# Kernel tuning notes

Measured on AMD Instinct MI355X. Metric: run time of the kernel, lower is better.

## Reference

```python
import jax, jax.numpy as jnp
import numpy as np

# Dimensions (match init_kwargs / input_specs)
B, C, H, W = 4, 64, 96, 96
G = 4                # groups of the deformable conv
K = 3                # kernel size
PAD, STRIDE, DIL = 1, 1, 1
KK = K * K


def setup_inputs() -> dict:
    key = jax.random.key(0)
    k1, k2, k3, k4 = jax.random.split(key, 4)
    x = jax.random.normal(k1, (B, C, H, W), jnp.float32)
    # offset-predicting conv: Conv2d(C -> 2*K*K, 3x3), kaiming-ish scale
    w_off = jax.random.normal(k2, (2 * KK, C, K, K), jnp.float32) / np.sqrt(C * KK)
    b_off = jax.random.normal(k3, (2 * KK,), jnp.float32) * 0.01
    # deformable conv weight: [C_out=C, C_in/groups, K, K], bias=False
    w_def = jax.random.normal(k4, (C, C // G, K, K), jnp.float32) / np.sqrt((C // G) * KK)
    return {"x": x, "w_off": w_off, "b_off": b_off, "w_def": w_def}


def _offset_conv(x, w, b):
    y = jax.lax.conv_general_dilated(
        x, w,
        window_strides=(STRIDE, STRIDE),
        padding=((PAD, PAD), (PAD, PAD)),
        rhs_dilation=(DIL, DIL),
        dimension_numbers=("NCHW", "OIHW", "NCHW"))
    return y + b[None, :, None, None]


def _deform_conv2d(x, offset, w_def):
    """torchvision.ops.DeformConv2d (mask=None, bias=None) semantics.

    x:      [B, C, H, W]
    offset: [B, 2*K*K, Ho, Wo]  channel layout (dy_k, dx_k) per kernel tap k=ki*K+kj
    w_def:  [C_out, C_in//G, K, K]
    """
    Bb, Cc, Hh, Ww = x.shape
    Ho, Wo = offset.shape[2], offset.shape[3]
    off = offset.reshape(Bb, KK, 2, Ho, Wo)  # [..., 0]=dy, [..., 1]=dx

    # Base sampling grid per kernel tap: p0 + p_k  -> [KK, Ho, Wo]
    taps = jnp.arange(K, dtype=jnp.float32) * DIL
    base_y = jnp.arange(Ho, dtype=jnp.float32) * STRIDE - PAD  # [Ho]
    base_x = jnp.arange(Wo, dtype=jnp.float32) * STRIDE - PAD  # [Wo]
    gy = (taps[:, None, None, None] + base_y[None, None, :, None])  # [K,1,Ho,1]
    gx = (taps[None, :, None, None] + base_x[None, None, None, :])  # [1,K,1,Wo]
    gy = jnp.broadcast_to(gy, (K, K, Ho, Wo)).reshape(KK, Ho, Wo)
    gx = jnp.broadcast_to(gx, (K, K, Ho, Wo)).reshape(KK, Ho, Wo)

    ys = gy[None] + off[:, :, 0]  # [B, KK, Ho, Wo]
    xs = gx[None] + off[:, :, 1]

    y0 = jnp.floor(ys)
    x0 = jnp.floor(xs)
    wy1 = ys - y0
    wx1 = xs - x0
    wy0 = 1.0 - wy1
    wx0 = 1.0 - wx1
    y0i = y0.astype(jnp.int32)
    x0i = x0.astype(jnp.int32)

    x_flat = x.reshape(Bb, Cc, Hh * Ww)

    def corner(iy, ix, wgt):
        # zero padding outside the image: mask invalid corners
        valid = (iy >= 0) & (iy < Hh) & (ix >= 0) & (ix < Ww)
        idx = jnp.clip(iy, 0, Hh - 1) * Ww + jnp.clip(ix, 0, Ww - 1)  # [B,KK,Ho,Wo]
        g = jnp.take_along_axis(x_flat, idx.reshape(Bb, -1)[:, None, :], axis=2)
        g = g.reshape(Bb, Cc, KK, Ho, Wo)
        return g * (wgt * valid)[:, None]  # broadcast over channels

    sampled = (corner(y0i,     x0i,     wy0 * wx0)
             + corner(y0i,     x0i + 1, wy0 * wx1)
             + corner(y0i + 1, x0i,     wy1 * wx0)
             + corner(y0i + 1, x0i + 1, wy1 * wx1))  # [B,C,KK,Ho,Wo]

    # grouped 9-tap contraction
    s = sampled.reshape(Bb, G, Cc // G, KK, Ho, Wo)
    wv = w_def.reshape(G, w_def.shape[0] // G, Cc // G, KK)  # [G, out/g, in/g, KK]
    out = jnp.einsum("bgckhw,gdck->bgdhw", s, wv)
    return out.reshape(Bb, w_def.shape[0], Ho, Wo)


def reference(x, w_off, b_off, w_def):
    offset = _offset_conv(x, w_off, b_off)
    return _deform_conv2d(x, offset, w_def)
```

## Files before the change

kernel.cpp:

```cpp
#include <hip/hip_runtime.h>
#include <hip/hip_bf16.h>

#define Bn   4
#define Cn   64
#define Hn   96
#define Wn   96
#define Gn   4
#define CGn  16
#define KKn  9
#define NOFF 18
#define HWn  (Hn*Wn)
#define PW   98
#define XH_PIX (PW*PW)

#define OFF_BASE  0
#define AWF_BASE  (Bn*HWn*NOFF)
#define WMF_BASE  (AWF_BASE + 9216)
#define XH_BASE   (WMF_BASE + 5120)
#define XG_BASE   (XH_BASE + 1229312)

typedef __attribute__((ext_vector_type(8))) short short8v;
typedef __attribute__((ext_vector_type(4))) float f32x4;
typedef __attribute__((ext_vector_type(2))) float f32x2;
typedef __attribute__((ext_vector_type(4))) unsigned int uint4v;
typedef unsigned short ushort_t;

__device__ inline short f2bs(float v) {
    __hip_bfloat16 h = __float2bfloat16(v);
    return *reinterpret_cast<short*>(&h);
}
__device__ inline unsigned pack2bf(float lo, float hi) {
    return (unsigned)(ushort_t)f2bs(lo) | ((unsigned)(ushort_t)f2bs(hi) << 16);
}

#define NTRB (Bn * (HWn / 64))
__global__ __launch_bounds__(256) void prep_all(
    const float* __restrict__ x, const float* __restrict__ w_off,
    const float* __restrict__ w_def, float* __restrict__ ws)
{
    __shared__ float t[64][65];
    if (blockIdx.x < NTRB) {
        const int nb = HWn / 64;
        const int b  = blockIdx.x / nb;
        const int p0 = (blockIdx.x % nb) * 64;
        ushort_t* xh = (ushort_t*)(ws + XH_BASE);
        ushort_t* xg = (ushort_t*)(ws + XG_BASE);
        for (int i = threadIdx.x; i < 64 * 64; i += 256) {
            const int c = i >> 6, l = i & 63;
            t[c][l] = x[(b * Cn + c) * HWn + p0 + l];
        }
        __syncthreads();
        for (int i = threadIdx.x; i < 64 * 32; i += 256) {
            const int l = i >> 5, cp = i & 31;
            const int pos = p0 + l;
            const int ho = pos / Wn, wo = pos % Wn;
            const unsigned pk = pack2bf(t[cp * 2][l], t[cp * 2 + 1][l]);
            *(unsigned*)(xh + ((size_t)b * XH_PIX + (ho + 1) * PW + wo + 1) * Cn
                             + cp * 2) = pk;
            const int g = cp >> 3, pg = cp & 7;
            *(unsigned*)(xg + ((size_t)(b * Gn + g) * HWn + pos) * CGn
                             + pg * 2) = pk;
        }
        return;
    }
    const int i = (blockIdx.x - NTRB) * 256 + threadIdx.x;
    const int NA = 18 * 2 * 16 * 4 * 8;
    const int NW = Gn * 5 * CGn * 4 * 8;
    if (i < NA) {
        const int jj  = i & 7;
        const int q   = (i >> 3) & 3;
        const int row = (i >> 5) & 15;
        const int tt  = (i >> 9) & 1;
        const int s   = i >> 10;
        const int u   = s * 4 + q;
        const int k   = u % 9, co = u / 9;
        const int ci  = co * 8 + jj;
        const int o   = tt * 16 + row;
        const float v = (o < NOFF) ? w_off[(o * Cn + ci) * KKn + k] : 0.f;
        ((__hip_bfloat16*)(ws + AWF_BASE))[i] = __float2bfloat16(v);
    } else if (i < NA + NW) {
        const int j  = i - NA;
        const int jj = j & 7;
        const int q  = (j >> 3) & 3;
        const int d  = (j >> 5) & 15;
        const int kp = (j >> 9) % 5;
        const int g  = j / 2560;
        const int c  = (q & 1) * 8 + jj;
        const int k  = 2 * kp + (q >> 1);
        const float v = (k < KKn) ? w_def[((g * CGn + d) * CGn + c) * KKn + k] : 0.f;
        ((__hip_bfloat16*)(ws + WMF_BASE))[j] = __float2bfloat16(v);
    } else {
        const int hidx = i - (NA + NW);
        if (hidx < Bn * 388) {
            const int b = hidx / 388;
            const int h = hidx % 388;
            int py, px;
            if (h < 98)       { py = 0;           px = h;        }
            else if (h < 196) { py = 97;          px = h - 98;   }
            else if (h < 292) { py = h - 196 + 1; px = 0;        }
            else              { py = h - 292 + 1; px = 97;       }
            f32x4 z = {0.f, 0.f, 0.f, 0.f};
            f32x4* p = (f32x4*)((ushort_t*)(ws + XH_BASE)
                       + ((size_t)b * XH_PIX + py * PW + px) * Cn);
            #pragma unroll
            for (int j2 = 0; j2 < 8; j2++) p[j2] = z;
        }
    }
}

__global__ __launch_bounds__(256) void offset_conv_v4(
    const float* __restrict__ ws, const float* __restrict__ bias,
    float* __restrict__ offs)
{
    const int bid = (blockIdx.x & 7) * 72 + (blockIdx.x >> 3);
    const int b = bid / 144;
    const int r = bid % 144;
    const int wave = threadIdx.x >> 6;
    const int lane = threadIdx.x & 63;
    const int pr = lane & 15, q = lane >> 4;
    const int pos0 = r * 64 + wave * 16;
    const int pos = pos0 + pr;
    const int ho = pos / Wn, wo = pos % Wn;
    const unsigned basep = (unsigned)(ho * PW + wo) * 128u;

    const ushort_t* xhb = (const ushort_t*)(ws + XH_BASE) + (size_t)b * XH_PIX * Cn;
    const ushort_t* awf = (const ushort_t*)(ws + AWF_BASE);
    const unsigned pa = (unsigned)(pr * 64 + q * 16);

    f32x4 bi4 = *(const f32x4*)(bias + q * 4);
    f32x2 bi2 = *(const f32x2*)(bias + 16);
    asm volatile("" : "+v"(bi4));
    asm volatile("" : "+v"(bi2));
    asm volatile("s_waitcnt vmcnt(0)" ::: "memory");
    __builtin_amdgcn_sched_barrier(0);

    short8v bfr[6], a0f[6], a1f[6];
    int kk = q, co = 0;
    f32x4 acc0 = {0.f,0.f,0.f,0.f}, acc1 = {0.f,0.f,0.f,0.f};

#define OISSUE(S) { \
    const int ki = kk / 3, kj = kk % 3; \
    const unsigned voff = basep + (unsigned)(ki * PW + kj) * 128u + (unsigned)co * 16u; \
    asm volatile("global_load_dwordx4 %0, %1, %2" : "=v"(bfr[(S)%6]) : "v"(voff), "s"(xhb)); \
    const unsigned aoff = pa + (unsigned)(S) * 2048u; \
    asm volatile("global_load_dwordx4 %0, %1, %2" : "=v"(a0f[(S)%6]) : "v"(aoff), "s"(awf)); \
    asm volatile("global_load_dwordx4 %0, %1, %2" : "=v"(a1f[(S)%6]) : "v"(aoff + 1024u), "s"(awf)); \
    kk += 4; const int cy_ = (kk >= 9) ? 1 : 0; co += cy_; kk -= cy_ * 9; }

#define OCONS(S, N) { \
    asm volatile("s_waitcnt vmcnt(" #N ")" ::: "memory"); \
    __builtin_amdgcn_sched_barrier(0); \
    acc0 = __builtin_amdgcn_mfma_f32_16x16x32_bf16(a0f[(S)%6], bfr[(S)%6], acc0, 0, 0, 0); \
    acc1 = __builtin_amdgcn_mfma_f32_16x16x32_bf16(a1f[(S)%6], bfr[(S)%6], acc1, 0, 0, 0); }

    OISSUE(0) OISSUE(1) OISSUE(2) OISSUE(3) OISSUE(4) OISSUE(5)
    OCONS(0, 15) OISSUE(6)
    OCONS(1, 15) OISSUE(7)
    OCONS(2, 15) OISSUE(8)
    OCONS(3, 15) OISSUE(9)
    OCONS(4, 15) OISSUE(10)
    OCONS(5, 15) OISSUE(11)
    OCONS(6, 15) OISSUE(12)
    OCONS(7, 15) OISSUE(13)
    OCONS(8, 15) OISSUE(14)
    OCONS(9, 15) OISSUE(15)
    OCONS(10, 15) OISSUE(16)
    OCONS(11, 15) OISSUE(17)
    OCONS(12, 15)
    OCONS(13, 12)
    OCONS(14, 9)
    OCONS(15, 6)
    OCONS(16, 3)
    OCONS(17, 0)
#undef OISSUE
#undef OCONS

    float* dst = offs + (size_t)(b * HWn + pos0 + pr) * NOFF + q * 4;
    f32x2 s01; s01.x = acc0[0] + bi4.x; s01.y = acc0[1] + bi4.y;
    f32x2 s23; s23.x = acc0[2] + bi4.z; s23.y = acc0[3] + bi4.w;
    *(f32x2*)dst = s01;
    *(f32x2*)(dst + 2) = s23;
    if (q == 0) {
        f32x2 s67; s67.x = acc1[0] + bi2.x; s67.y = acc1[1] + bi2.y;
        *(f32x2*)(offs + (size_t)(b * HWn + pos0 + pr) * NOFF + 16) = s67;
    }
}

#define GLOAD4(dst, off_) \
    asm volatile("global_load_dwordx4 %0, %1, %2" \
                 : "=v"(dst) : "v"(off_), "s"(xgb))

__global__ __launch_bounds__(256) void deform_v9(
    const float* __restrict__ ws, float* __restrict__ out)
{
    const float* __restrict__ off2 = ws + OFF_BASE;
    const short8v* __restrict__ wmf = (const short8v*)(ws + WMF_BASE);

    const int bid = (blockIdx.x & 7) * 288 + (blockIdx.x >> 3);
    const int nbb = HWn / 64;
    const int bg  = bid / nbb;
    const int g   = bg & (Gn - 1);
    const int b   = bg >> 2;
    const int wave = threadIdx.x >> 6;
    const int lane = threadIdx.x & 63;
    const int pr   = lane & 15;
    const int q    = lane >> 4;
    const int half = q & 1;
    const int tp   = q >> 1;
    const int pos0 = (bid % nbb) * 64 + wave * 16;
    const int pos  = pos0 + pr;
    const int ho = pos / Wn, wo = pos % Wn;

    const f32x2* op2 = (const f32x2*)(off2 + (size_t)(b * HWn + pos) * NOFF);
    f32x2 o2[5];
    #pragma unroll
    for (int kp = 0; kp < 5; kp++) {
        int kq = 2 * kp + tp; if (kq > 8) kq = 8;
        o2[kp] = op2[kq];
    }
    short8v a[5];
    #pragma unroll
    for (int kp = 0; kp < 5; kp++)
        a[kp] = wmf[((g * 5 + kp) * CGn + pr) * 4 + q];

    const ushort_t* xgb = (const ushort_t*)(ws + XG_BASE)
                        + (size_t)(b * Gn + g) * HWn * CGn;
    const unsigned hoff = (unsigned)half * 16u;

    #pragma unroll
    for (int kp = 0; kp < 5; kp++) {
        asm volatile("" : "+v"(o2[kp]));
        asm volatile("" : "+v"(a[kp]));
    }
    asm volatile("s_waitcnt vmcnt(0)" ::: "memory");
    __builtin_amdgcn_sched_barrier(0);

    float cwt[5][4];
    f32x4 dat[5][4];

#define PAIRSETUP(KP)                                                      \
  {                                                                        \
    const int k  = 2 * (KP) + tp;                                          \
    const int ki = k / 3, kj = k - 3 * ki;                                 \
    const float m = (k <= 8) ? 1.f : 0.f;                                  \
    const float ysf = (float)(ho - 1 + ki) + o2[KP].x;                     \
    const float xsf = (float)(wo - 1 + kj) + o2[KP].y;                     \
    const float y0f = floorf(ysf), x0f = floorf(xsf);                      \
    const int   y0  = (int)y0f,    x0  = (int)x0f;                         \
    const float wy1 = ysf - y0f, wx1 = xsf - x0f;                          \
    const float wy0 = 1.f - wy1, wx0 = 1.f - wx1;                          \
    const bool vy0 = (y0 >= 0)  && (y0 < Hn);                              \
    const bool vy1 = (y0 >= -1) && (y0 < Hn - 1);                          \
    const bool vx0 = (x0 >= 0)  && (x0 < Wn);                              \
    const bool vx1 = (x0 >= -1) && (x0 < Wn - 1);                          \
    const int cy0 = min(max(y0,     0), Hn - 1);                           \
    const int cy1 = min(max(y0 + 1, 0), Hn - 1);                           \
    const int cx0 = min(max(x0,     0), Wn - 1);                           \
    const int cx1 = min(max(x0 + 1, 0), Wn - 1);                           \
    cwt[KP][0] = m * wy0 * wx0 * ((vy0 && vx0) ? 1.f : 0.f);               \
    cwt[KP][1] = m * wy0 * wx1 * ((vy0 && vx1) ? 1.f : 0.f);               \
    cwt[KP][2] = m * wy1 * wx0 * ((vy1 && vx0) ? 1.f : 0.f);               \
    cwt[KP][3] = m * wy1 * wx1 * ((vy1 && vx1) ? 1.f : 0.f);               \
    const unsigned v00 = (unsigned)(cy0 * Wn + cx0) * 32u + hoff;          \
    const unsigned v01 = (unsigned)(cy0 * Wn + cx1) * 32u + hoff;          \
    const unsigned v10 = (unsigned)(cy1 * Wn + cx0) * 32u + hoff;          \
    const unsigned v11 = (unsigned)(cy1 * Wn + cx1) * 32u + hoff;          \
    GLOAD4(dat[KP][0], v00);                                               \
    GLOAD4(dat[KP][1], v01);                                               \
    GLOAD4(dat[KP][2], v10);                                               \
    GLOAD4(dat[KP][3], v11);                                               \
  }

    PAIRSETUP(0); PAIRSETUP(1); PAIRSETUP(2);

    f32x4 acc = {0.f, 0.f, 0.f, 0.f};

    #pragma unroll
    for (int kp = 0; kp < 5; kp++) {
        if (kp <= 2)      asm volatile("s_waitcnt vmcnt(8)" ::: "memory");
        else if (kp == 3) asm volatile("s_waitcnt vmcnt(4)" ::: "memory");
        else              asm volatile("s_waitcnt vmcnt(0)" ::: "memory");
        __builtin_amdgcn_sched_barrier(0);

        float s[8] = {0.f,0.f,0.f,0.f,0.f,0.f,0.f,0.f};
        #pragma unroll
        for (int c4 = 0; c4 < 4; c4++) {
            const float w = cwt[kp][c4];
            const uint4v u = *reinterpret_cast<const uint4v*>(&dat[kp][c4]);
            #pragma unroll
            for (int w2 = 0; w2 < 4; w2++) {
                unsigned lo = u[w2] << 16;
                unsigned hi = u[w2] & 0xffff0000u;
                s[2*w2]   += w * *reinterpret_cast<float*>(&lo);
                s[2*w2+1] += w * *reinterpret_cast<float*>(&hi);
            }
        }
        short8v fr;
        #pragma unroll
        for (int j = 0; j < 8; j++) fr[j] = f2bs(s[j]);
        acc = __builtin_amdgcn_mfma_f32_16x16x32_bf16(a[kp], fr, acc, 0, 0, 0);

        if (kp == 0) PAIRSETUP(3);
        if (kp == 1) PAIRSETUP(4);
    }

    float* op = out + (size_t)(b * Cn + g * CGn) * HWn + pos0;
    #pragma unroll
    for (int r = 0; r < 4; r++)
        op[(q * 4 + r) * HWn + pr] = acc[r];
}

extern "C" void kernel_launch(void* const* d_in, const int* in_sizes, int n_in,
                              void* d_out, int out_size, void* d_ws, size_t ws_size,
                              hipStream_t stream) {
    const float* x     = (const float*)d_in[0];
    const float* w_off = (const float*)d_in[1];
    const float* b_off = (const float*)d_in[2];
    const float* w_def = (const float*)d_in[3];
    float* out = (float*)d_out;
    float* ws  = (float*)d_ws;

    const int n_pack = 18432 + 10240;
    const int nblk = NTRB + n_pack / 256 + 7;
    prep_all<<<nblk, 256, 0, stream>>>(x, w_off, w_def, ws);

    offset_conv_v4<<<576, 256, 0, stream>>>(ws, b_off, ws + OFF_BASE);

    deform_v9<<<Bn * Gn * (HWn / 64), 256, 0, stream>>>(ws, out);
}
```

Measured before the change: 43.98 us.

## Merge padded and grouped bf16 copies of x into one halo-padded group-planar layout

The prep kernel now writes a single bf16 copy of x in a per-(batch,group) planar layout with a one-pixel zero halo, instead of both a padded channel-last copy and an unpadded grouped copy. The offset conv indexes this layout by plane and channel half, and the deform kernel reads it using padded coordinates. This halves prep write traffic and workspace footprint. The deform kernel also shrinks its gather buffers from 5 to 3 ring slots and adds scheduling barriers, which lowers register pressure at the cost of stricter instruction ordering.

Result: faster. 37.25 us (median of 3 runs) (-15.3%).

```diff
diff --git a/kernel.cpp b/kernel.cpp
--- a/kernel.cpp
+++ b/kernel.cpp
@@ -12,12 +12,12 @@
 #define HWn  (Hn*Wn)
 #define PW   98
 #define XH_PIX (PW*PW)
+#define PLANE_B (XH_PIX * CGn * 2)
 
 #define OFF_BASE  0
 #define AWF_BASE  (Bn*HWn*NOFF)
 #define WMF_BASE  (AWF_BASE + 9216)
-#define XH_BASE   (WMF_BASE + 5120)
-#define XG_BASE   (XH_BASE + 1229312)
+#define XGH_BASE  (WMF_BASE + 5120)
 
 typedef __attribute__((ext_vector_type(8))) short short8v;
 typedef __attribute__((ext_vector_type(4))) float f32x4;
@@ -34,6 +34,7 @@
 }
 
 #define NTRB (Bn * (HWn / 64))
+#define NHALO (Bn * Gn * 388)
 __global__ __launch_bounds__(256) void prep_all(
     const float* __restrict__ x, const float* __restrict__ w_off,
     const float* __restrict__ w_def, float* __restrict__ ws)
@@ -43,8 +44,7 @@
         const int nb = HWn / 64;
         const int b  = blockIdx.x / nb;
         const int p0 = (blockIdx.x % nb) * 64;
-        ushort_t* xh = (ushort_t*)(ws + XH_BASE);
-        ushort_t* xg = (ushort_t*)(ws + XG_BASE);
+        ushort_t* xgh = (ushort_t*)(ws + XGH_BASE);
         for (int i = threadIdx.x; i < 64 * 64; i += 256) {
             const int c = i >> 6, l = i & 63;
             t[c][l] = x[(b * Cn + c) * HWn + p0 + l];
@@ -55,11 +55,9 @@
             const int pos = p0 + l;
             const int ho = pos / Wn, wo = pos % Wn;
             const unsigned pk = pack2bf(t[cp * 2][l], t[cp * 2 + 1][l]);
-            *(unsigned*)(xh + ((size_t)b * XH_PIX + (ho + 1) * PW + wo + 1) * Cn
-                             + cp * 2) = pk;
             const int g = cp >> 3, pg = cp & 7;
-            *(unsigned*)(xg + ((size_t)(b * Gn + g) * HWn + pos) * CGn
-                             + pg * 2) = pk;
+            *(unsigned*)(xgh + ((size_t)(b * Gn + g) * XH_PIX
+                                + (ho + 1) * PW + (wo + 1)) * CGn + pg * 2) = pk;
         }
         return;
     }
@@ -91,8 +89,8 @@
         ((__hip_bfloat16*)(ws + WMF_BASE))[j] = __float2bfloat16(v);
     } else {
         const int hidx = i - (NA + NW);
-        if (hidx < Bn * 388) {
-            const int b = hidx / 388;
+        if (hidx < NHALO) {
+            const int plane = hidx / 388;
             const int h = hidx % 388;
             int py, px;
             if (h < 98)       { py = 0;           px = h;        }
@@ -100,10 +98,9 @@
             else if (h < 292) { py = h - 196 + 1; px = 0;        }
             else              { py = h - 292 + 1; px = 97;       }
             f32x4 z = {0.f, 0.f, 0.f, 0.f};
-            f32x4* p = (f32x4*)((ushort_t*)(ws + XH_BASE)
-                       + ((size_t)b * XH_PIX + py * PW + px) * Cn);
-            #pragma unroll
-            for (int j2 = 0; j2 < 8; j2++) p[j2] = z;
+            f32x4* p = (f32x4*)((ushort_t*)(ws + XGH_BASE)
+                       + ((size_t)plane * XH_PIX + py * PW + px) * CGn);
+            p[0] = z; p[1] = z;
         }
     }
 }
@@ -121,9 +118,10 @@
     const int pos0 = r * 64 + wave * 16;
     const int pos = pos0 + pr;
     const int ho = pos / Wn, wo = pos % Wn;
-    const unsigned basep = (unsigned)(ho * PW + wo) * 128u;
-
-    const ushort_t* xhb = (const ushort_t*)(ws + XH_BASE) + (size_t)b * XH_PIX * Cn;
+    const unsigned basep = (unsigned)(ho * PW + wo) * 32u;
+
+    const ushort_t* xhb = (const ushort_t*)(ws + XGH_BASE)
+                        + (size_t)b * Gn * XH_PIX * CGn;
     const ushort_t* awf = (const ushort_t*)(ws + AWF_BASE);
     const unsigned pa = (unsigned)(pr * 64 + q * 16);
 
@@ -140,7 +138,8 @@
 
 #define OISSUE(S) { \
     const int ki = kk / 3, kj = kk % 3; \
-    const unsigned voff = basep + (unsigned)(ki * PW + kj) * 128u + (unsigned)co * 16u; \
+    const unsigned voff = (unsigned)(co >> 1) * (unsigned)PLANE_B + basep \
+                        + (unsigned)(ki * PW + kj) * 32u + (unsigned)(co & 1) * 16u; \
     asm volatile("global_load_dwordx4 %0, %1, %2" : "=v"(bfr[(S)%6]) : "v"(voff), "s"(xhb)); \
     const unsigned aoff = pa + (unsigned)(S) * 2048u; \
     asm volatile("global_load_dwordx4 %0, %1, %2" : "=v"(a0f[(S)%6]) : "v"(aoff), "s"(awf)); \
@@ -190,7 +189,7 @@
     asm volatile("global_load_dwordx4 %0, %1, %2" \
                  : "=v"(dst) : "v"(off_), "s"(xgb))
 
-__global__ __launch_bounds__(256) void deform_v9(
+__global__ __launch_bounds__(256) void deform_v12(
     const float* __restrict__ ws, float* __restrict__ out)
 {
     const float* __restrict__ off2 = ws + OFF_BASE;
@@ -223,8 +222,8 @@
     for (int kp = 0; kp < 5; kp++)
         a[kp] = wmf[((g * 5 + kp) * CGn + pr) * 4 + q];
 
-    const ushort_t* xgb = (const ushort_t*)(ws + XG_BASE)
-                        + (size_t)(b * Gn + g) * HWn * CGn;
+    const ushort_t* xgb = (const ushort_t*)(ws + XGH_BASE)
+                        + (size_t)(b * Gn + g) * XH_PIX * CGn;
     const unsigned hoff = (unsigned)half * 16u;
 
     #pragma unroll
@@ -235,8 +234,8 @@
     asm volatile("s_waitcnt vmcnt(0)" ::: "memory");
     __builtin_amdgcn_sched_barrier(0);
 
-    float cwt[5][4];
-    f32x4 dat[5][4];
+    float cwt[3][4];
+    f32x4 dat[3][4];
 
 #define PAIRSETUP(KP)                                                      \
   {                                                                        \
@@ -257,18 +256,18 @@
     const int cy1 = min(max(y0 + 1, 0), Hn - 1);                           \
     const int cx0 = min(max(x0,     0), Wn - 1);                           \
     const int cx1 = min(max(x0 + 1, 0), Wn - 1);                           \
-    cwt[KP][0] = m * wy0 * wx0 * ((vy0 && vx0) ? 1.f : 0.f);               \
-    cwt[KP][1] = m * wy0 * wx1 * ((vy0 && vx1) ? 1.f : 0.f);               \
-    cwt[KP][2] = m * wy1 * wx0 * ((vy1 && vx0) ? 1.f : 0.f);               \
-    cwt[KP][3] = m * wy1 * wx1 * ((vy1 && vx1) ? 1.f : 0.f);               \
-    const unsigned v00 = (unsigned)(cy0 * Wn + cx0) * 32u + hoff;          \
-    const unsigned v01 = (unsigned)(cy0 * Wn + cx1) * 32u + hoff;          \
-    const unsigned v10 = (unsigned)(cy1 * Wn + cx0) * 32u + hoff;          \
-    const unsigned v11 = (unsigned)(cy1 * Wn + cx1) * 32u + hoff;          \
-    GLOAD4(dat[KP][0], v00);                                               \
-    GLOAD4(dat[KP][1], v01);                                               \
-    GLOAD4(dat[KP][2], v10);                                               \
-    GLOAD4(dat[KP][3], v11);                                               \
+    cwt[(KP)%3][0] = m * wy0 * wx0 * ((vy0 && vx0) ? 1.f : 0.f);           \
+    cwt[(KP)%3][1] = m * wy0 * wx1 * ((vy0 && vx1) ? 1.f : 0.f);           \
+    cwt[(KP)%3][2] = m * wy1 * wx0 * ((vy1 && vx0) ? 1.f : 0.f);           \
+    cwt[(KP)%3][3] = m * wy1 * wx1 * ((vy1 && vx1) ? 1.f : 0.f);           \
+    const unsigned v00 = (unsigned)((cy0 + 1) * PW + cx0 + 1) * 32u + hoff; \
+    const unsigned v01 = (unsigned)((cy0 + 1) * PW + cx1 + 1) * 32u + hoff; \
+    const unsigned v10 = (unsigned)((cy1 + 1) * PW + cx0 + 1) * 32u + hoff; \
+    const unsigned v11 = (unsigned)((cy1 + 1) * PW + cx1 + 1) * 32u + hoff; \
+    GLOAD4(dat[(KP)%3][0], v00);                                           \
+    GLOAD4(dat[(KP)%3][1], v01);                                           \
+    GLOAD4(dat[(KP)%3][2], v10);                                           \
+    GLOAD4(dat[(KP)%3][3], v11);                                           \
   }
 
     PAIRSETUP(0); PAIRSETUP(1); PAIRSETUP(2);
@@ -282,11 +281,12 @@
         else              asm volatile("s_waitcnt vmcnt(0)" ::: "memory");
         __builtin_amdgcn_sched_barrier(0);
 
+        const int sl = kp % 3;
         float s[8] = {0.f,0.f,0.f,0.f,0.f,0.f,0.f,0.f};
         #pragma unroll
         for (int c4 = 0; c4 < 4; c4++) {
-            const float w = cwt[kp][c4];
-            const uint4v u = *reinterpret_cast<const uint4v*>(&dat[kp][c4]);
+            const float w = cwt[sl][c4];
+            const uint4v u = *reinterpret_cast<const uint4v*>(&dat[sl][c4]);
             #pragma unroll
             for (int w2 = 0; w2 < 4; w2++) {
                 unsigned lo = u[w2] << 16;
@@ -300,8 +300,8 @@
         for (int j = 0; j < 8; j++) fr[j] = f2bs(s[j]);
         acc = __builtin_amdgcn_mfma_f32_16x16x32_bf16(a[kp], fr, acc, 0, 0, 0);
 
-        if (kp == 0) PAIRSETUP(3);
-        if (kp == 1) PAIRSETUP(4);
+        if (kp == 0) { __builtin_amdgcn_sched_barrier(0); PAIRSETUP(3); }
+        if (kp == 1) { __builtin_amdgcn_sched_barrier(0); PAIRSETUP(4); }
     }
 
     float* op = out + (size_t)(b * Cn + g * CGn) * HWn + pos0;
@@ -320,11 +320,11 @@
     float* out = (float*)d_out;
     float* ws  = (float*)d_ws;
 
-    const int n_pack = 18432 + 10240;
-    const int nblk = NTRB + n_pack / 256 + 7;
+    const int n_rest = 18432 + 10240 + NHALO;
+    const int nblk = NTRB + (n_rest + 255) / 256;
     prep_all<<<nblk, 256, 0, stream>>>(x, w_off, w_def, ws);
 
     offset_conv_v4<<<576, 256, 0, stream>>>(ws, b_off, ws + OFF_BASE);
 
-    deform_v9<<<Bn * Gn * (HWn / 64), 256, 0, stream>>>(ws, out);
-}
+    deform_v12<<<Bn * Gn * (HWn / 64), 256, 0, stream>>>(ws, out);
+}
```
